# Performance work log

Measured on AMD Instinct MI355X. Metric: run time of the kernel, lower is better.

## Reference

```python
import jax, jax.numpy as jnp
import numpy as np

HEADS = 8

def setup_inputs() -> dict:
    key = jax.random.key(0)
    ks = jax.random.split(key, 6)
    b, c, w, h = 4, 512, 48, 48
    qc, vc = 512, 512
    s = 1.0 / np.sqrt(c)  # orthogonal-init-like scale for 1x1 conv weights
    return {
        "x": jax.random.normal(ks[0], (b, c, w, h), dtype=jnp.float32),
        "Wq": jax.random.normal(ks[1], (qc, c), dtype=jnp.float32) * s,
        "Wk": jax.random.normal(ks[2], (qc, c), dtype=jnp.float32) * s,
        "Wv": jax.random.normal(ks[3], (vc, c), dtype=jnp.float32) * s,
        "Wsc": jax.random.normal(ks[4], (vc, c), dtype=jnp.float32) * s,
        "gamma": jax.random.normal(ks[5], (1, vc, 1, 1), dtype=jnp.float32),
    }


def reference(x, Wq, Wk, Wv, Wsc, gamma):
    b, c, w, h = x.shape
    n = w * h
    dq = Wq.shape[0] // HEADS
    dv = Wv.shape[0] // HEADS
    # 1x1 convs are channel matmuls
    q = jnp.einsum('bchw,oc->bohw', x, Wq).reshape(b, HEADS, dq, n)
    k = jnp.einsum('bchw,oc->bohw', x, Wk).reshape(b, HEADS, dq, n)
    v = jnp.einsum('bchw,oc->bohw', x, Wv).reshape(b, HEADS, dv, n)
    # attention scores over spatial tokens (no scaling in original)
    attn = jax.nn.softmax(jnp.einsum('bhdn,bhdm->bhnm', q, k), axis=-1)
    out = jnp.einsum('bhnm,bhdm->bnhd', attn, v)  # (b, n, heads, dv)
    out = out.reshape(b, w, h, HEADS * dv).transpose(0, 3, 1, 2)  # head-major channels
    sc = jnp.einsum('bchw,oc->bohw', x, Wsc)
    return gamma * out + sc
```

## Files before the change

### kernel.cpp

```cpp
#include <hip/hip_runtime.h>

#define HEADS 8
static constexpr int BSZ = 4;
static constexpr int CCH = 512;
static constexpr int NSP = 2304;
static constexpr int DH  = 64;

typedef _Float16 f16x8 __attribute__((ext_vector_type(8)));
typedef float f32x4 __attribute__((ext_vector_type(4)));
typedef float f32x16 __attribute__((ext_vector_type(16)));
typedef int i32x4 __attribute__((ext_vector_type(4)));
typedef unsigned short u16;
typedef unsigned int u32;

__device__ __forceinline__ u16 f2h(float f) {
  _Float16 h = (_Float16)f;
  return __builtin_bit_cast(u16, h);
}

__device__ __forceinline__ float fexp2(float x) {
  return __builtin_amdgcn_exp2f(x);
}

__device__ __forceinline__ void gl_lds16(const void* g, void* l) {
  __builtin_amdgcn_global_load_lds(
      (const __attribute__((address_space(1))) u32*)g,
      (__attribute__((address_space(3))) u32*)l, 16, 0, 0);
}

__global__ void k_cvt_w(const float* __restrict__ w0, const float* __restrict__ w1,
                        const float* __restrict__ w2, const float* __restrict__ w3,
                        u16* __restrict__ dst) {
  int wsel = blockIdx.y;
  const float* src = wsel == 0 ? w0 : wsel == 1 ? w1 : wsel == 2 ? w2 : w3;
  int i = (blockIdx.x * 256 + threadIdx.x) * 4;
  float4 v = *(const float4*)(src + i);
  ushort4 o;
  o.x = f2h(v.x); o.y = f2h(v.y); o.z = f2h(v.z); o.w = f2h(v.w);
  *(ushort4*)(dst + (size_t)wsel * CCH * CCH + i) = o;
}

__global__ void k_cvt_x(const float* __restrict__ x, u16* __restrict__ xT) {
  __shared__ u16 t[64][66];
  int b = blockIdx.z, c0 = blockIdx.y * 64, n0 = blockIdx.x * 64;
  int col = threadIdx.x & 63, rb = threadIdx.x >> 6;
#pragma unroll
  for (int rr = 0; rr < 16; rr++) {
    int r = rr * 4 + rb;
    t[r][col] = f2h(x[((size_t)b * CCH + c0 + r) * NSP + n0 + col]);
  }
  __syncthreads();
#pragma unroll
  for (int rr = 0; rr < 16; rr++) {
    int r = rr * 4 + rb;
    xT[((size_t)b * NSP + n0 + r) * CCH + c0 + col] = t[col][r];
  }
}

__global__ __launch_bounds__(256) void k_proj(const u16* __restrict__ Wall,
    const u16* __restrict__ xT, u16* __restrict__ Qo, u16* __restrict__ Ko,
    u16* __restrict__ Vo, float* __restrict__ SCo) {
  __shared__ u16 smem[17408];
  u16* At = smem;
  u16* Bt = smem + 8192;
  int z = blockIdx.z, b = z >> 2, wsel = z & 3;
  int o0 = blockIdx.y * 128, n0 = blockIdx.x * 128;
  int tid = threadIdx.x, lane = tid & 63, wv = tid >> 6;
  int wr = wv >> 1, wc = wv & 1;
  const u16* Asrc = Wall + (size_t)wsel * CCH * CCH + (size_t)o0 * CCH;
  const u16* Bsrc = xT + ((size_t)b * NSP + n0) * CCH;
  f32x4 acc[4][4] = {};
  for (int kc = 0; kc < CCH; kc += 64) {
    __syncthreads();
#pragma unroll
    for (int i = 0; i < 4; i++) {
      int ch = (wv * 4 + i) * 64 + lane;
      int row = ch >> 3, cc = ch & 7;
      gl_lds16(Asrc + (size_t)row * CCH + kc + ((cc ^ (row & 7)) << 3), At + (wv * 4 + i) * 512);
      gl_lds16(Bsrc + (size_t)row * CCH + kc + ((cc ^ (row & 7)) << 3), Bt + (wv * 4 + i) * 512);
    }
    __syncthreads();
#pragma unroll
    for (int ks = 0; ks < 2; ks++) {
      f16x8 af[4], bfr[4];
#pragma unroll
      for (int f = 0; f < 4; f++) {
        int orow = wr * 64 + f * 16 + (lane & 15);
        int nrow = wc * 64 + f * 16 + (lane & 15);
        int k8 = (lane >> 4) + ks * 4;
        af[f]  = *(const f16x8*)(At + orow * 64 + ((k8 ^ (orow & 7)) << 3));
        bfr[f] = *(const f16x8*)(Bt + nrow * 64 + ((k8 ^ (nrow & 7)) << 3));
      }
#pragma unroll
      for (int i = 0; i < 4; i++)
#pragma unroll
        for (int j = 0; j < 4; j++)
          acc[i][j] = __builtin_amdgcn_mfma_f32_16x16x32_f16(af[i], bfr[j], acc[i][j], 0, 0, 0);
    }
  }
  if (wsel >= 2) {
#pragma unroll
    for (int i = 0; i < 4; i++)
#pragma unroll
      for (int j = 0; j < 4; j++)
#pragma unroll
        for (int r = 0; r < 4; r++) {
          int o = o0 + wr * 64 + i * 16 + ((lane >> 4) << 2) + r;
          int n = n0 + wc * 64 + j * 16 + (lane & 15);
          size_t idx = ((size_t)b * CCH + o) * NSP + n;
          if (wsel == 3) SCo[idx] = acc[i][j][r];
          else           Vo[idx]  = f2h(acc[i][j][r]);
        }
  } else {
    __syncthreads();
    u16* stash = smem;
    float qs = (wsel == 0) ? 1.4426950408889634f : 1.0f;
#pragma unroll
    for (int i = 0; i < 4; i++)
#pragma unroll
      for (int j = 0; j < 4; j++)
#pragma unroll
        for (int r = 0; r < 4; r++) {
          int ol = wr * 64 + i * 16 + ((lane >> 4) << 2) + r;
          int nl = wc * 64 + j * 16 + (lane & 15);
          stash[nl * 136 + ol] = f2h(acc[i][j][r] * qs);
        }
    __syncthreads();
    u16* dst = wsel ? Ko : Qo;
    int hl = tid >> 7, nn = tid & 127;
    int h = (o0 >> 6) + hl;
    size_t base = ((size_t)(b * HEADS + h) * NSP + n0 + nn) * DH;
#pragma unroll
    for (int c2 = 0; c2 < 8; c2++)
      *(int4*)(dst + base + c2 * 8) = *(const int4*)(stash + nn * 136 + hl * 64 + c2 * 8);
  }
}

__global__ __launch_bounds__(128) void k_attn(const u16* __restrict__ Qw,
    const u16* __restrict__ Kw, const u16* __restrict__ Vw,
    const float* __restrict__ gamma, float* __restrict__ out) {
  __shared__ u16 smem[8192];
  int qt = blockIdx.x, bh = blockIdx.y;
  int b = bh >> 3, h = bh & 7;
  int tid = threadIdx.x, lane = tid & 63, wv = tid >> 6;
  int l31 = lane & 31, hi = lane >> 5;
  int q0w = qt * 64 + wv * 32;
  const u16* Ksrc = Kw + (size_t)bh * NSP * DH;
  const u16* Vsrc = Vw + ((size_t)b * CCH + h * DH) * NSP;
  u16* Kb0 = smem;
  u16* Kb1 = smem + 4096;

  int ch0 = tid, ch1 = 128 + tid;
  int mk0 = ch0 >> 3, pk0 = ch0 & 7, mk1 = ch1 >> 3, pk1 = ch1 & 7;
  const u16* kc0 = Ksrc + mk0 * DH + ((pk0 ^ (mk0 & 7)) << 3);
  const u16* kc1 = Ksrc + mk1 * DH + ((pk1 ^ (mk1 & 7)) << 3);
  int dv0 = ch0 >> 2, pv0 = ch0 & 3, dv1 = ch1 >> 2, pv1 = ch1 & 3;
  const u16* vc0 = Vsrc + dv0 * NSP + ((pv0 ^ ((dv0 >> 1) & 3)) << 3);
  const u16* vc1 = Vsrc + dv1 * NSP + ((pv1 ^ ((dv1 >> 1) & 3)) << 3);

#define STAGE(KB)                                  \
  do {                                             \
    gl_lds16(kc0, (KB) + ch0 * 8);                 \
    gl_lds16(kc1, (KB) + ch1 * 8);                 \
    gl_lds16(vc0, (KB) + 2048 + ch0 * 8);          \
    gl_lds16(vc1, (KB) + 2048 + ch1 * 8);          \
    kc0 += 32 * DH; kc1 += 32 * DH;                \
    vc0 += 32; vc1 += 32;                          \
  } while (0)

  int kswz = l31 & 7, vswz = (l31 >> 1) & 3;
  int kro = l31 * 64;
  int ko[4], vo[2];
#pragma unroll
  for (int kd = 0; kd < 4; kd++) ko[kd] = ((2 * kd + hi) ^ kswz) << 3;
#pragma unroll
  for (int s = 0; s < 2; s++) vo[s] = ((2 * s + hi) ^ vswz) << 3;
  int vr0 = l31 * 32, vr1 = (32 + l31) * 32;

  f16x8 qf[4];
  const u16* Qbase = Qw + ((size_t)bh * NSP + q0w + l31) * DH + hi * 8;
#pragma unroll
  for (int kd = 0; kd < 4; kd++)
    qf[kd] = *(const f16x8*)(Qbase + kd * 16);

  float mrun = -1e30f, lrun = 0.f;
  f32x16 acc0 = {}, acc1 = {};

#define COMPUTE(KB)                                                          \
  do {                                                                       \
    const u16* Kc = (KB);                                                    \
    const u16* Vc = (KB) + 2048;                                             \
    f32x16 s0 = {};                                                          \
    __builtin_amdgcn_s_setprio(1);                                           \
    _Pragma("unroll")                                                        \
    for (int kd = 0; kd < 4; kd++) {                                         \
      f16x8 k0 = *(const f16x8*)(Kc + kro + ko[kd]);                         \
      s0 = __builtin_amdgcn_mfma_f32_32x32x16_f16(k0, qf[kd], s0, 0, 0, 0);  \
    }                                                                        \
    __builtin_amdgcn_s_setprio(0);                                           \
    float m0a = fmaxf(fmaxf(s0[0], s0[1]), s0[2]);                           \
    float m0b = fmaxf(fmaxf(s0[3], s0[4]), s0[5]);                           \
    float m0c = fmaxf(fmaxf(s0[6], s0[7]), s0[8]);                           \
    float m0d = fmaxf(fmaxf(s0[9], s0[10]), s0[11]);                         \
    float m0e = fmaxf(fmaxf(s0[12], s0[13]), s0[14]);                        \
    float tm = fmaxf(fmaxf(fmaxf(m0a, m0b), fmaxf(m0c, m0d)),                \
                     fmaxf(m0e, s0[15]));                                    \
    tm = fmaxf(tm, __shfl_xor(tm, 32));                                      \
    if (__any(tm > mrun + 11.5f)) {                                          \
      float mnew = fmaxf(mrun, tm);                                          \
      float scl = fexp2(mrun - mnew);                                        \
      mrun = mnew;                                                           \
      lrun *= scl;                                                           \
      _Pragma("unroll")                                                      \
      for (int r = 0; r < 16; r++) {                                         \
        float sq = __shfl(scl, (r & 3) + 8 * (r >> 2) + 4 * hi);             \
        acc0[r] *= sq;                                                       \
        acc1[r] *= sq;                                                       \
      }                                                                      \
    }                                                                        \
    float ts = 0.f;                                                          \
    u32 P2[4][2];                                                            \
    _Pragma("unroll")                                                        \
    for (int s2 = 0; s2 < 4; s2++)                                           \
      _Pragma("unroll")                                                      \
      for (int c = 0; c < 2; c++) {                                          \
        float a = fexp2(s0[4 * s2 + 2 * c] - mrun);                          \
        float bb = fexp2(s0[4 * s2 + 2 * c + 1] - mrun);                     \
        ts += a + bb;                                                        \
        P2[s2][c] = __builtin_bit_cast(u32, __builtin_amdgcn_cvt_pkrtz(a, bb)); \
      }                                                                      \
    ts += __shfl_xor(ts, 32);                                                \
    lrun += ts;                                                              \
    _Pragma("unroll")                                                        \
    for (int s = 0; s < 2; s++) {                                            \
      int x0 = (int)P2[2 * s][0], y0 = (int)P2[2 * s + 1][0];                \
      int x1 = (int)P2[2 * s][1], y1 = (int)P2[2 * s + 1][1];                \
      asm("v_permlane32_swap_b32 %0, %1" : "+v"(x0), "+v"(y0));              \
      asm("v_permlane32_swap_b32 %0, %1" : "+v"(x1), "+v"(y1));              \
      f16x8 pa = __builtin_bit_cast(f16x8, (i32x4){x0, x1, y0, y1});         \
      __builtin_amdgcn_s_setprio(1);                                         \
      {                                                                      \
        f16x8 vb = *(const f16x8*)(Vc + vr0 + vo[s]);                        \
        acc0 = __builtin_amdgcn_mfma_f32_32x32x16_f16(pa, vb, acc0, 0, 0, 0);\
      }                                                                      \
      {                                                                      \
        f16x8 vb = *(const f16x8*)(Vc + vr1 + vo[s]);                        \
        acc1 = __builtin_amdgcn_mfma_f32_32x32x16_f16(pa, vb, acc1, 0, 0, 0);\
      }                                                                      \
      __builtin_amdgcn_s_setprio(0);                                         \
    }                                                                        \
  } while (0)

  STAGE(Kb0);
  __syncthreads();
  for (int it2 = 0; it2 < 36; it2++) {
    STAGE(Kb1);
    COMPUTE(Kb0);
    __syncthreads();
    if (it2 < 35) STAGE(Kb0);
    COMPUTE(Kb1);
    __syncthreads();
  }

  float inv = 1.0f / lrun;
  float invq[16];
#pragma unroll
  for (int r = 0; r < 16; r++)
    invq[r] = __shfl(inv, (r & 3) + 8 * (r >> 2) + 4 * hi);
  size_t outbase = ((size_t)b * CCH + h * DH) * NSP;
#pragma unroll
  for (int dblk = 0; dblk < 2; dblk++) {
    int d = dblk * 32 + l31;
    float g = gamma[h * DH + d];
    float* orow = out + outbase + (size_t)d * NSP + q0w;
#pragma unroll
    for (int s2 = 0; s2 < 4; s2++) {
      int n = 8 * s2 + 4 * hi;
      f32x4 o;
#pragma unroll
      for (int t = 0; t < 4; t++) {
        int r = 4 * s2 + t;
        float a = dblk ? acc1[r] : acc0[r];
        o[t] = a * invq[r] * g;
      }
      f32x4 sc = *(const f32x4*)(orow + n);
      *(f32x4*)(orow + n) = o + sc;
    }
  }
#undef STAGE
#undef COMPUTE
}

extern "C" void kernel_launch(void* const* d_in, const int* in_sizes, int n_in,
                              void* d_out, int out_size, void* d_ws, size_t ws_size,
                              hipStream_t stream) {
  const float* x     = (const float*)d_in[0];
  const float* Wq    = (const float*)d_in[1];
  const float* Wk    = (const float*)d_in[2];
  const float* Wv    = (const float*)d_in[3];
  const float* Wsc   = (const float*)d_in[4];
  const float* gamma = (const float*)d_in[5];
  float* out = (float*)d_out;

  u16* xT   = (u16*)d_ws;
  u16* Wall = xT + (size_t)BSZ * NSP * CCH;
  u16* Qw   = Wall + (size_t)4 * CCH * CCH;
  u16* Kw   = Qw + (size_t)BSZ * CCH * NSP;
  u16* Vw   = Kw + (size_t)BSZ * CCH * NSP;

  hipLaunchKernelGGL(k_cvt_w, dim3(CCH * CCH / 1024, 4), dim3(256), 0, stream,
                     Wq, Wk, Wv, Wsc, Wall);
  hipLaunchKernelGGL(k_cvt_x, dim3(NSP / 64, CCH / 64, BSZ), dim3(256), 0, stream, x, xT);
  hipLaunchKernelGGL(k_proj, dim3(NSP / 128, CCH / 128, BSZ * 4), dim3(256), 0, stream,
                     Wall, xT, Qw, Kw, Vw, out);
  hipLaunchKernelGGL(k_attn, dim3(NSP / 64, BSZ * HEADS), dim3(128), 0, stream,
                     Qw, Kw, Vw, gamma, out);
}
```

Before: 167.5 us.

## Split attention KV range across two wave groups and merge softmax partials

The attention block grows to 512 threads covering 128 queries, with two groups of four waves each processing alternating 32-key chunks (a split-KV scheme inside the block). Partial accumulators and running max/sum from the second group go through LDS and are merged by the first group with rescaling before the output epilogue. Each block now loads each K/V tile once for 4 query waves, halving K/V staging traffic per query, and the iteration count per wave halves. The cost is a final LDS merge, larger LDS use, fewer blocks (576), and block-wide syncs across 8 waves.

```diff
diff --git a/kernel.cpp b/kernel.cpp
--- a/kernel.cpp
+++ b/kernel.cpp
@@ -136,36 +136,32 @@
   }
 }
 
-__global__ __launch_bounds__(128) void k_attn(const u16* __restrict__ Qw,
+__global__ __launch_bounds__(512) void k_attn(const u16* __restrict__ Qw,
     const u16* __restrict__ Kw, const u16* __restrict__ Vw,
     const float* __restrict__ gamma, float* __restrict__ out) {
-  __shared__ u16 smem[8192];
+  __shared__ u16 smem[17408];
   int qt = blockIdx.x, bh = blockIdx.y;
   int b = bh >> 3, h = bh & 7;
   int tid = threadIdx.x, lane = tid & 63, wv = tid >> 6;
   int l31 = lane & 31, hi = lane >> 5;
-  int q0w = qt * 64 + wv * 32;
+  int qh = wv & 3, tp = wv >> 2;
+  int gid = tid & 255;
+  int q0w = qt * 128 + qh * 32;
   const u16* Ksrc = Kw + (size_t)bh * NSP * DH;
   const u16* Vsrc = Vw + ((size_t)b * CCH + h * DH) * NSP;
-  u16* Kb0 = smem;
-  u16* Kb1 = smem + 4096;
-
-  int ch0 = tid, ch1 = 128 + tid;
-  int mk0 = ch0 >> 3, pk0 = ch0 & 7, mk1 = ch1 >> 3, pk1 = ch1 & 7;
-  const u16* kc0 = Ksrc + mk0 * DH + ((pk0 ^ (mk0 & 7)) << 3);
-  const u16* kc1 = Ksrc + mk1 * DH + ((pk1 ^ (mk1 & 7)) << 3);
-  int dv0 = ch0 >> 2, pv0 = ch0 & 3, dv1 = ch1 >> 2, pv1 = ch1 & 3;
-  const u16* vc0 = Vsrc + dv0 * NSP + ((pv0 ^ ((dv0 >> 1) & 3)) << 3);
-  const u16* vc1 = Vsrc + dv1 * NSP + ((pv1 ^ ((dv1 >> 1) & 3)) << 3);
-
-#define STAGE(KB)                                  \
+  u16* PB = smem + tp * 8192;
+
+  int mk = gid >> 3, pk = gid & 7;
+  const u16* kc = Ksrc + (tp * 32 + mk) * DH + ((pk ^ (mk & 7)) << 3);
+  int dv = gid >> 2, pv = gid & 3;
+  const u16* vc = Vsrc + (size_t)dv * NSP + tp * 32 + ((pv ^ ((dv >> 1) & 3)) << 3);
+
+#define STAGE(c)                                   \
   do {                                             \
-    gl_lds16(kc0, (KB) + ch0 * 8);                 \
-    gl_lds16(kc1, (KB) + ch1 * 8);                 \
-    gl_lds16(vc0, (KB) + 2048 + ch0 * 8);          \
-    gl_lds16(vc1, (KB) + 2048 + ch1 * 8);          \
-    kc0 += 32 * DH; kc1 += 32 * DH;                \
-    vc0 += 32; vc1 += 32;                          \
+    gl_lds16(kc, PB + (c) * 4096 + gid * 8);       \
+    gl_lds16(vc, PB + (c) * 4096 + 2048 + gid * 8);\
+    kc += 64 * DH;                                 \
+    vc += 64;                                      \
   } while (0)
 
   int kswz = l31 & 7, vswz = (l31 >> 1) & 3;
@@ -186,10 +182,10 @@
   float mrun = -1e30f, lrun = 0.f;
   f32x16 acc0 = {}, acc1 = {};
 
-#define COMPUTE(KB)                                                          \
+#define COMPUTE(c)                                                           \
   do {                                                                       \
-    const u16* Kc = (KB);                                                    \
-    const u16* Vc = (KB) + 2048;                                             \
+    const u16* Kc = PB + (c) * 4096;                                         \
+    const u16* Vc = Kc + 2048;                                               \
     f32x16 s0 = {};                                                          \
     __builtin_amdgcn_s_setprio(1);                                           \
     _Pragma("unroll")                                                        \
@@ -223,11 +219,11 @@
     _Pragma("unroll")                                                        \
     for (int s2 = 0; s2 < 4; s2++)                                           \
       _Pragma("unroll")                                                      \
-      for (int c = 0; c < 2; c++) {                                          \
-        float a = fexp2(s0[4 * s2 + 2 * c] - mrun);                          \
-        float bb = fexp2(s0[4 * s2 + 2 * c + 1] - mrun);                     \
+      for (int c2 = 0; c2 < 2; c2++) {                                       \
+        float a = fexp2(s0[4 * s2 + 2 * c2] - mrun);                         \
+        float bb = fexp2(s0[4 * s2 + 2 * c2 + 1] - mrun);                    \
         ts += a + bb;                                                        \
-        P2[s2][c] = __builtin_bit_cast(u32, __builtin_amdgcn_cvt_pkrtz(a, bb)); \
+        P2[s2][c2] = __builtin_bit_cast(u32, __builtin_amdgcn_cvt_pkrtz(a, bb)); \
       }                                                                      \
     ts += __shfl_xor(ts, 32);                                                \
     lrun += ts;                                                              \
@@ -251,40 +247,64 @@
     }                                                                        \
   } while (0)
 
-  STAGE(Kb0);
+  STAGE(0);
   __syncthreads();
-  for (int it2 = 0; it2 < 36; it2++) {
-    STAGE(Kb1);
-    COMPUTE(Kb0);
-    __syncthreads();
-    if (it2 < 35) STAGE(Kb0);
-    COMPUTE(Kb1);
-    __syncthreads();
-  }
-
-  float inv = 1.0f / lrun;
-  float invq[16];
-#pragma unroll
-  for (int r = 0; r < 16; r++)
-    invq[r] = __shfl(inv, (r & 3) + 8 * (r >> 2) + 4 * hi);
-  size_t outbase = ((size_t)b * CCH + h * DH) * NSP;
-#pragma unroll
-  for (int dblk = 0; dblk < 2; dblk++) {
-    int d = dblk * 32 + l31;
-    float g = gamma[h * DH + d];
-    float* orow = out + outbase + (size_t)d * NSP + q0w;
-#pragma unroll
-    for (int s2 = 0; s2 < 4; s2++) {
-      int n = 8 * s2 + 4 * hi;
-      f32x4 o;
-#pragma unroll
-      for (int t = 0; t < 4; t++) {
-        int r = 4 * s2 + t;
-        float a = dblk ? acc1[r] : acc0[r];
-        o[t] = a * invq[r] * g;
+  for (int i2 = 0; i2 < 18; i2++) {
+    STAGE(1);
+    COMPUTE(0);
+    __syncthreads();
+    if (i2 < 17) STAGE(0);
+    COMPUTE(1);
+    __syncthreads();
+  }
+
+  float* sf = (float*)smem;
+  if (tp) {
+#pragma unroll
+    for (int r = 0; r < 16; r++) {
+      sf[qh * 2048 + r * 64 + lane] = acc0[r];
+      sf[qh * 2048 + (16 + r) * 64 + lane] = acc1[r];
+    }
+    if (lane < 32) {
+      sf[8192 + qh * 64 + l31] = mrun;
+      sf[8192 + qh * 64 + 32 + l31] = lrun;
+    }
+  }
+  __syncthreads();
+  if (!tp) {
+    float mb = sf[8192 + qh * 64 + l31];
+    float lb = sf[8192 + qh * 64 + 32 + l31];
+    float M = fmaxf(mrun, mb);
+    float fa = fexp2(mrun - M), fb = fexp2(mb - M);
+    float linv = 1.0f / (lrun * fa + lb * fb);
+    fa *= linv; fb *= linv;
+    float faq[16], fbq[16];
+#pragma unroll
+    for (int r = 0; r < 16; r++) {
+      int qloc = (r & 3) + 8 * (r >> 2) + 4 * hi;
+      faq[r] = __shfl(fa, qloc);
+      fbq[r] = __shfl(fb, qloc);
+    }
+    size_t outbase = ((size_t)b * CCH + h * DH) * NSP;
+#pragma unroll
+    for (int dblk = 0; dblk < 2; dblk++) {
+      int d = dblk * 32 + l31;
+      float g = gamma[h * DH + d];
+      float* orow = out + outbase + (size_t)d * NSP + q0w;
+#pragma unroll
+      for (int s2 = 0; s2 < 4; s2++) {
+        int n = 8 * s2 + 4 * hi;
+        f32x4 o;
+#pragma unroll
+        for (int t = 0; t < 4; t++) {
+          int r = 4 * s2 + t;
+          float oa = dblk ? acc1[r] : acc0[r];
+          float ob = sf[qh * 2048 + (dblk * 16 + r) * 64 + lane];
+          o[t] = (oa * faq[r] + ob * fbq[r]) * g;
+        }
+        f32x4 sc = *(const f32x4*)(orow + n);
+        *(f32x4*)(orow + n) = o + sc;
       }
-      f32x4 sc = *(const f32x4*)(orow + n);
-      *(f32x4*)(orow + n) = o + sc;
     }
   }
 #undef STAGE
@@ -313,6 +333,6 @@
   hipLaunchKernelGGL(k_cvt_x, dim3(NSP / 64, CCH / 64, BSZ), dim3(256), 0, stream, x, xT);
   hipLaunchKernelGGL(k_proj, dim3(NSP / 128, CCH / 128, BSZ * 4), dim3(256), 0, stream,
                      Wall, xT, Qw, Kw, Vw, out);
-  hipLaunchKernelGGL(k_attn, dim3(NSP / 64, BSZ * HEADS), dim3(128), 0, stream,
+  hipLaunchKernelGGL(k_attn, dim3(NSP / 128, BSZ * HEADS), dim3(512), 0, stream,
                      Qw, Kw, Vw, gamma, out);
 }
```

After: 144.4 us. 1.16x faster.
